# Kernel optimization log

Measured on AMD Instinct MI355X. Metric: run time of the kernel, lower is better.

The kernel has to match this reference:

```python
import jax, jax.numpy as jnp
import numpy as np

LN_EPS = 1e-5
FD_EPS = 1e-3   # cfg.fd_eps
MAX_ITER = 2    # cfg.max_iter; early-exit on tol is a host-side .item() check in torch, omitted for jit (fixed iterations)


def _block(w1, b1, w2, b2, g, beta, x):
    # pre-LN MLP residual block: x + W2 @ gelu(W1 @ LN(x))
    mu = jnp.mean(x, axis=-1, keepdims=True)
    var = jnp.var(x, axis=-1, keepdims=True)
    xn = (x - mu) * jax.lax.rsqrt(var + LN_EPS) * g + beta
    h = jax.nn.gelu(xn @ w1 + b1)
    return x + h @ w2 + b2

# apply block_l to state_l for all l at once: (L,B,T,C) -> (L,B,T,C)
_vblock = jax.vmap(_block, in_axes=(0, 0, 0, 0, 0, 0, 0))


def _scan_solve(As, bs):
    # solve x_l = A_l * x_{l-1} + b_l with x_0 = b_0 (A_0 unused), O(log L)
    def combine(e1, e2):
        A1, c1 = e1
        A2, c2 = e2
        return A2 * A1, A2 * c1 + c2
    _, xs = jax.lax.associative_scan(combine, (As, bs), axis=0)
    return xs


def setup_inputs() -> dict:
    key = jax.random.key(0)
    ks = jax.random.split(key, 3)
    L, B, T, C, F = 12, 2, 512, 768, 3072
    return {
        "x0": jax.random.normal(ks[0], (B, T, C), jnp.float32),
        "w1": jax.random.normal(ks[1], (L, C, F), jnp.float32) * 0.02,
        "b1": jnp.zeros((L, F), jnp.float32),
        "w2": jax.random.normal(ks[2], (L, F, C), jnp.float32) * 0.02,
        "b2": jnp.zeros((L, C), jnp.float32),
        "g": jnp.ones((L, C), jnp.float32),
        "beta": jnp.zeros((L, C), jnp.float32),
    }


def reference(x0, w1, b1, w2, b2, g, beta):
    L = w1.shape[0]
    # picard warmstart: states[l+1] = block_l(x0) (computed under torch.no_grad)
    warm = jax.lax.stop_gradient(
        _vblock(w1, b1, w2, b2, g, beta, jnp.broadcast_to(x0, (L,) + x0.shape)))
    states = jnp.concatenate([x0[None], warm], axis=0)  # (L+1, B, T, C)
    key = jax.random.key(42)
    for it in range(MAX_ITER):
        # residuals r_l = block_l(x_l) - x_{l+1}
        outs = _vblock(w1, b1, w2, b2, g, beta, states[:-1])
        res = outs - states[1:]
        # quasi-DEER FD diagonal Jacobian (Rademacher probe, under no_grad)
        sg = jax.lax.stop_gradient(states[:-1])
        v = jnp.sign(jax.random.normal(jax.random.fold_in(key, it), sg.shape, jnp.float32))
        op = _vblock(w1, b1, w2, b2, g, beta, sg + FD_EPS * v)
        om = _vblock(w1, b1, w2, b2, g, beta, sg - FD_EPS * v)
        diag_J = jax.lax.stop_gradient((op - om) / (2.0 * FD_EPS) * v)
        # damping k=0 for quasi-deer -> A_l = diag_J_l, b_l = r_l
        delta = _scan_solve(diag_J, res)  # (L, B, T, C)
        states = states.at[1:].add(delta)
    return states[-1]
```

## Files before the change

kernel.cpp:

```cpp
#include <hip/hip_runtime.h>
#include <hip/hip_bf16.h>
#include <stdint.h>


typedef __bf16 bf16;
typedef __bf16 bf16x8 __attribute__((ext_vector_type(8)));
typedef float f32x4 __attribute__((ext_vector_type(4)));

#define LAY_A   1572864
#define LAY_W   2359296
#define LAY_Z   6291456
#define LAY_S   786432

#define GLDS16(gp, lp) __builtin_amdgcn_global_load_lds(                      \
    (const __attribute__((address_space(1))) void*)(gp),                      \
    (__attribute__((address_space(3))) void*)(lp), 16, 0, 0)

#define WAITVM(N) asm volatile("s_waitcnt vmcnt(%0)" :: "n"(N) : "memory")
#define CFENCE()  asm volatile("" ::: "memory")

#define TF_ROT(x0, x1, n) { x0 += x1; x1 = (x1 << n) | (x1 >> (32 - n)); x1 ^= x0; }
__host__ __device__ __forceinline__ void threefry2x32(
    uint32_t k1, uint32_t k2, uint32_t c0, uint32_t c1, uint32_t& o0, uint32_t& o1)
{
  const uint32_t ks2 = k1 ^ k2 ^ 0x1BD11BDAu;
  uint32_t x0 = c0 + k1, x1 = c1 + k2;
  TF_ROT(x0,x1,13) TF_ROT(x0,x1,15) TF_ROT(x0,x1,26) TF_ROT(x0,x1,6)
  x0 += k2;  x1 += ks2 + 1u;
  TF_ROT(x0,x1,17) TF_ROT(x0,x1,29) TF_ROT(x0,x1,16) TF_ROT(x0,x1,24)
  x0 += ks2; x1 += k1 + 2u;
  TF_ROT(x0,x1,13) TF_ROT(x0,x1,15) TF_ROT(x0,x1,26) TF_ROT(x0,x1,6)
  x0 += k1;  x1 += k2 + 3u;
  TF_ROT(x0,x1,17) TF_ROT(x0,x1,29) TF_ROT(x0,x1,16) TF_ROT(x0,x1,24)
  x0 += k2;  x1 += ks2 + 4u;
  TF_ROT(x0,x1,13) TF_ROT(x0,x1,15) TF_ROT(x0,x1,26) TF_ROT(x0,x1,6)
  x0 += ks2; x1 += k1 + 5u;
  o0 = x0; o1 = x1;
}

__global__ __launch_bounds__(256) void transpose_kernel(
    const float* __restrict__ w, bf16* __restrict__ wt, int R, int Cc)
{
  __shared__ float tile[32][33];
  const int l = blockIdx.z;
  const float* wp = w + (size_t)l * R * Cc;
  bf16* wtp = wt + (size_t)l * R * Cc;
  const int c0 = blockIdx.x * 32;
  const int r0 = blockIdx.y * 32;
  const int tx = threadIdx.x & 31, ty = threadIdx.x >> 5;
  #pragma unroll
  for (int q = 0; q < 4; ++q)
    tile[ty + q * 8][tx] = wp[(size_t)(r0 + ty + q * 8) * Cc + c0 + tx];
  __syncthreads();
  #pragma unroll
  for (int q = 0; q < 4; ++q)
    wtp[(size_t)(c0 + ty + q * 8) * R + r0 + tx] = (bf16)tile[tx][ty + q * 8];
}

__device__ __forceinline__ void gelu2(float z, float& h, float& dg)
{
  const float z2 = z * z;
  const float u = 0.7978845608028654f * (z + 0.044715f * z2 * z);
  const float t = tanhf(u);
  h = 0.5f * z * (1.f + t);
  dg = 0.5f * (1.f + t) +
       0.5f * z * (1.f - t * t) * 0.7978845608028654f * (1.f + 0.134145f * z2);
}

template <int MODE>
__global__ __launch_bounds__(512, 2) void gemm_dbuf(
    const bf16* __restrict__ Abase, const bf16* __restrict__ Bbase,
    bf16* __restrict__ zh_out, float* __restrict__ states,
    float* __restrict__ resA, const bf16* __restrict__ vbuf,
    const float* __restrict__ bias1, const float* __restrict__ b2,
    const float* __restrict__ x0, int Mt)
{
  constexpr int LDAB  = (MODE <= 1) ? 768 : 3072;
  constexpr int NKT   = (MODE <= 1) ? 12 : 48;
  constexpr int NTN   = (MODE <= 1) ? 12 : ((MODE == 2) ? 3 : 6);
  constexpr int TN    = (MODE == 3) ? 128 : 256;
  constexpr int NFRAG = TN / 64;
  constexpr int ACH   = 32;
  constexpr int BCH   = TN / 8;
  constexpr int NCH   = (ACH + BCH) / 8;
  constexpr int ABYTES = 32768;
  constexpr int TILE  = ABYTES + BCH * 1024;
  constexpr size_t LSA = (MODE <= 1) ? LAY_A : LAY_Z;

  __shared__ __align__(16) char lds[2][TILE];

  const int tid  = threadIdx.x;
  const int lane = tid & 63;
  const int wid  = tid >> 6;
  const int wr   = wid >> 2;
  const int wc   = wid & 3;
  const int r16  = lane & 15;
  const int hi   = lane >> 4;

  const int nwg = gridDim.x;
  const int bid = blockIdx.x;
  const int swz = (bid & 7) * (nwg >> 3) + (bid >> 3);
  const int per_l = Mt * NTN;
  const int l   = swz / per_l;
  const int rr_ = swz - l * per_l;
  const int mt  = rr_ / NTN;
  const int nt  = rr_ - mt * NTN;
  const int m0  = mt * 256, n0 = nt * TN;

  const bf16* A = Abase + (size_t)l * LSA   + (size_t)m0 * LDAB;
  const bf16* B = Bbase + (size_t)l * LAY_W + (size_t)n0 * LDAB;

  const int rsub = lane >> 3;
  const int c8   = (lane & 7) ^ rsub;
  auto STAGE = [&](char* dst, int kt) {
    #pragma unroll
    for (int j = 0; j < NCH; ++j) {
      const int chunk = j * 8 + wid;
      if (chunk < ACH) {
        const int row = chunk * 8 + rsub;
        GLDS16(A + (size_t)row * LDAB + kt + c8 * 8, dst + chunk * 1024);
      } else {
        const int row = (chunk - ACH) * 8 + rsub;
        GLDS16(B + (size_t)row * LDAB + kt + c8 * 8,
               dst + ABYTES + (chunk - ACH) * 1024);
      }
    }
  };

  f32x4 acc[8][NFRAG] = {};

  auto COMPUTE = [&](const char* buf) {
    const char* As = buf;
    const char* Bs = buf + ABYTES;
    const int xw = (r16 & 7) << 4;
    #pragma unroll
    for (int kk = 0; kk < 2; ++kk) {
      const int cb = kk * 64;
      bf16x8 bfrag[NFRAG];
      #pragma unroll
      for (int ni = 0; ni < NFRAG; ++ni) {
        const int rn = wc * (TN / 4) + ni * 16 + r16;
        bfrag[ni] = *(const bf16x8*)(Bs + rn * 128 + ((cb + hi * 16) ^ xw));
      }
      #pragma unroll
      for (int mh = 0; mh < 2; ++mh) {
        bf16x8 afrag[4];
        #pragma unroll
        for (int q = 0; q < 4; ++q) {
          const int rm = wr * 128 + (mh * 4 + q) * 16 + r16;
          afrag[q] = *(const bf16x8*)(As + rm * 128 + ((cb + hi * 16) ^ xw));
        }
        #pragma unroll
        for (int q = 0; q < 4; ++q)
          #pragma unroll
          for (int ni = 0; ni < NFRAG; ++ni)
            acc[mh * 4 + q][ni] = __builtin_amdgcn_mfma_f32_16x16x32_bf16(
                afrag[q], bfrag[ni], acc[mh * 4 + q][ni], 0, 0, 0);
      }
    }
  };

  STAGE(lds[0], 0);
  STAGE(lds[1], 64);
  WAITVM(NCH);
  __builtin_amdgcn_s_barrier();
  CFENCE();
  COMPUTE(lds[0]);
  #pragma unroll 1
  for (int t = 1; t < NKT; ++t) {
    CFENCE();
    __builtin_amdgcn_s_barrier();
    CFENCE();
    if (t + 1 < NKT) {
      STAGE(lds[(t + 1) & 1], (t + 1) * 64);
      WAITVM(NCH);
    } else {
      WAITVM(0);
    }
    __builtin_amdgcn_s_barrier();
    CFENCE();
    COMPUTE(lds[t & 1]);
  }

  #pragma unroll
  for (int mi = 0; mi < 8; ++mi) {
    const int row0 = m0 + wr * 128 + mi * 16 + hi * 4;
    #pragma unroll
    for (int ni = 0; ni < NFRAG; ++ni) {
      const int col = n0 + wc * (TN / 4) + ni * 16 + r16;
      if (MODE == 0) {
        bf16* Cp = zh_out + (size_t)l * LAY_Z;
        const float bias = bias1[l * 3072 + col];
        #pragma unroll
        for (int r = 0; r < 4; ++r) {
          float h, dg;
          gelu2(acc[mi][ni][r] + bias, h, dg);
          Cp[(size_t)(row0 + r) * 3072 + col] = (bf16)h;
        }
      } else if (MODE == 1) {
        bf16* Cp = zh_out + (size_t)l * LAY_Z;
        const float bias = bias1[l * 3072 + col];
        #pragma unroll
        for (int p = 0; p < 2; ++p) {
          float h, dg;
          gelu2(acc[mi][ni][2 * p] + bias, h, dg);
          Cp[(size_t)(row0 + 2 * p) * 3072 + col] = (bf16)h;
          Cp[(size_t)(row0 + 2 * p + 1) * 3072 + col] =
              (bf16)(dg * acc[mi][ni][2 * p + 1]);
        }
      } else if (MODE == 2) {
        float* Sp = states + (size_t)(l + 1) * LAY_S;
        const float bb = b2[l * 768 + col];
        #pragma unroll
        for (int r = 0; r < 4; ++r)
          Sp[(size_t)(row0 + r) * 768 + col] =
              acc[mi][ni][r] + bb + x0[(size_t)(row0 + r) * 768 + col];
      } else {
        float* Rp = resA + (size_t)l * LAY_A;
        const float bb = b2[l * 768 + col];
        #pragma unroll
        for (int p = 0; p < 2; ++p) {
          const int tok = (row0 >> 1) + p;
          Rp[(size_t)tok * 768 + col] = acc[mi][ni][2 * p] + bb
              + states[(size_t)l * LAY_S + (size_t)tok * 768 + col]
              - states[(size_t)(l + 1) * LAY_S + (size_t)tok * 768 + col];
          const float vv = (float)vbuf[(size_t)l * LAY_S +
                                       (size_t)tok * 768 + col];
          Rp[LAY_S + (size_t)tok * 768 + col] =
              1.0f + acc[mi][ni][2 * p + 1] * vv;
        }
      }
    }
  }
}

__global__ __launch_bounds__(256) void ln_warm_kernel(
    const float* __restrict__ x0, const float* __restrict__ g,
    const float* __restrict__ beta, bf16* __restrict__ a_buf)
{
  const int row = blockIdx.x * 4 + (threadIdx.x >> 6);
  const int lane = threadIdx.x & 63;
  const float* x = x0 + (size_t)row * 768;
  float xl[12];
  float s1 = 0.f, s2 = 0.f;
  #pragma unroll
  for (int j = 0; j < 12; ++j) {
    float t = x[lane + 64 * j];
    xl[j] = t; s1 += t; s2 += t * t;
  }
  #pragma unroll
  for (int off = 1; off < 64; off <<= 1) {
    s1 += __shfl_xor(s1, off);
    s2 += __shfl_xor(s2, off);
  }
  const float mu = s1 * (1.f / 768.f);
  const float var = s2 * (1.f / 768.f) - mu * mu;
  const float rstd = rsqrtf(var + 1e-5f);
  float xh[12];
  #pragma unroll
  for (int j = 0; j < 12; ++j) xh[j] = (xl[j] - mu) * rstd;
  for (int l = 0; l < 12; ++l) {
    const float* gp = g + l * 768;
    const float* bp = beta + l * 768;
    bf16* ap = a_buf + (size_t)l * LAY_A + (size_t)row * 768;
    #pragma unroll
    for (int j = 0; j < 12; ++j) {
      const int c = lane + 64 * j;
      ap[c] = (bf16)(xh[j] * gp[c] + bp[c]);
    }
  }
}

__global__ __launch_bounds__(256) void ln_iter_kernel(
    const float* __restrict__ states, bf16* __restrict__ vbuf,
    const float* __restrict__ g, const float* __restrict__ beta,
    bf16* __restrict__ a_buf, uint32_t k1, uint32_t k2)
{
  const int gr = blockIdx.x * 4 + (threadIdx.x >> 6);
  const int l = gr >> 10;
  const int row = gr & 1023;
  const int lane = threadIdx.x & 63;
  const float* x = states + (size_t)l * LAY_S + (size_t)row * 768;
  bf16* vp = vbuf + (size_t)gr * 768;
  float xl[12], vl[12];
  float s1 = 0.f, s2 = 0.f, sv = 0.f, sxv = 0.f;
  #pragma unroll
  for (int j = 0; j < 12; ++j) {
    const int c = lane + 64 * j;
    const float t = x[c];
    uint32_t o0, o1;
    threefry2x32(k1, k2, 0u, (uint32_t)gr * 768u + (uint32_t)c, o0, o1);
    const float u = ((o0 ^ o1) & 0x80000000u) ? 1.0f : -1.0f;
    vp[c] = (bf16)u;
    xl[j] = t; vl[j] = u;
    s1 += t; s2 += t * t; sv += u; sxv += t * u;
  }
  #pragma unroll
  for (int off = 1; off < 64; off <<= 1) {
    s1 += __shfl_xor(s1, off); s2 += __shfl_xor(s2, off);
    sv += __shfl_xor(sv, off); sxv += __shfl_xor(sxv, off);
  }
  const float mu = s1 * (1.f / 768.f);
  const float var = s2 * (1.f / 768.f) - mu * mu;
  const float rstd = rsqrtf(var + 1e-5f);
  const float mv = sv * (1.f / 768.f);
  const float mhv = rstd * (sxv * (1.f / 768.f) - mu * mv);
  const float* gp = g + l * 768;
  const float* bp = beta + l * 768;
  bf16* ap = a_buf + (size_t)l * LAY_A + (size_t)(2 * row) * 768;
  bf16* dp = ap + 768;
  #pragma unroll
  for (int j = 0; j < 12; ++j) {
    const int c = lane + 64 * j;
    const float xh = (xl[j] - mu) * rstd;
    ap[c] = (bf16)(xh * gp[c] + bp[c]);
    dp[c] = (bf16)(rstd * ((vl[j] - mv) - xh * mhv) * gp[c]);
  }
}

__global__ __launch_bounds__(256) void scan_kernel(
    const float* __restrict__ resA, float* __restrict__ states)
{
  const size_t i = (size_t)blockIdx.x * 256 + threadIdx.x;
  float run = resA[i];
  states[LAY_S + i] += run;
  #pragma unroll
  for (int l = 1; l < 12; ++l) {
    const float b  = resA[(size_t)l * LAY_A + i];
    const float Aa = resA[(size_t)l * LAY_A + LAY_S + i];
    run = b + Aa * run;
    states[(size_t)(l + 1) * LAY_S + i] += run;
  }
}

extern "C" void kernel_launch(void* const* d_in, const int* in_sizes, int n_in,
                              void* d_out, int out_size, void* d_ws, size_t ws_size,
                              hipStream_t stream)
{
  const float* x0   = (const float*)d_in[0];
  const float* w1   = (const float*)d_in[1];
  const float* b1   = (const float*)d_in[2];
  const float* w2   = (const float*)d_in[3];
  const float* b2   = (const float*)d_in[4];
  const float* g    = (const float*)d_in[5];
  const float* beta = (const float*)d_in[6];

  char* ws = (char*)d_ws;
  size_t off = 0;
  auto alloc = [&](size_t bytes) -> void* {
    void* p = ws + off;
    off += (bytes + 255) & ~(size_t)255;
    return p;
  };
  bf16*  w1t    = (bf16*)alloc(2ULL * 12 * LAY_W);
  bf16*  w2t    = (bf16*)alloc(2ULL * 12 * LAY_W);
  float* states = (float*)alloc(4ULL * 13 * LAY_S);
  bf16*  a_buf  = (bf16*)alloc(2ULL * 12 * LAY_A);
  bf16*  zh     = (bf16*)alloc(2ULL * 12 * LAY_Z);
  float* resA   = (float*)alloc(4ULL * 12 * LAY_A);
  bf16*  vbuf   = (bf16*)alloc(2ULL * 12 * LAY_S);

  transpose_kernel<<<dim3(96, 24, 12), 256, 0, stream>>>(w1, w1t, 768, 3072);
  transpose_kernel<<<dim3(24, 96, 12), 256, 0, stream>>>(w2, w2t, 3072, 768);
  hipMemcpyAsync(states, x0, 4ULL * LAY_S, hipMemcpyDeviceToDevice, stream);

  ln_warm_kernel<<<256, 256, 0, stream>>>(x0, g, beta, a_buf);
  gemm_dbuf<0><<<576, 512, 0, stream>>>(a_buf, w1t, zh, states, resA, vbuf,
                                        b1, b2, x0, 4);
  gemm_dbuf<2><<<144, 512, 0, stream>>>(zh, w2t, nullptr, states, resA, vbuf,
                                        b1, b2, x0, 4);

  for (int it = 0; it < 2; ++it) {
    uint32_t k1, k2;
    threefry2x32(0u, 42u, 0u, (uint32_t)it, k1, k2);
    ln_iter_kernel<<<3072, 256, 0, stream>>>(states, vbuf, g, beta, a_buf,
                                             k1, k2);
    gemm_dbuf<1><<<1152, 512, 0, stream>>>(a_buf, w1t, zh, states, resA, vbuf,
                                           b1, b2, x0, 8);
    gemm_dbuf<3><<<576, 512, 0, stream>>>(zh, w2t, nullptr, states, resA, vbuf,
                                          b1, b2, x0, 8);
    scan_kernel<<<3072, 256, 0, stream>>>(resA, states);
  }

  hipMemcpyAsync(d_out, states + 12ULL * LAY_S, 4ULL * LAY_S,
                 hipMemcpyDeviceToDevice, stream);
}
```

Baseline: 1.130 ms.

## Use 256x128 tiles for all GEMM modes with triple-buffered LDS pipeline

Every GEMM mode now uses a 256x128 output tile with a 4x2 wave layout (64x64 per wave). Grid sizes double for the modes that previously used 256-wide tiles. The LDS double buffer becomes a triple buffer that prefetches two k-tiles ahead, aiming to hide global load latency better and to raise occupancy and wave counts through smaller accumulator arrays. The cost is more A-tile reloads per output and more total LDS per block.

```diff
diff --git a/kernel.cpp b/kernel.cpp
--- a/kernel.cpp
+++ b/kernel.cpp
@@ -77,23 +77,21 @@
 {
   constexpr int LDAB  = (MODE <= 1) ? 768 : 3072;
   constexpr int NKT   = (MODE <= 1) ? 12 : 48;
-  constexpr int NTN   = (MODE <= 1) ? 12 : ((MODE == 2) ? 3 : 6);
-  constexpr int TN    = (MODE == 3) ? 128 : 256;
-  constexpr int NFRAG = TN / 64;
+  constexpr int NTN   = (MODE <= 1) ? 24 : 6;
   constexpr int ACH   = 32;
-  constexpr int BCH   = TN / 8;
+  constexpr int BCH   = 16;
   constexpr int NCH   = (ACH + BCH) / 8;
   constexpr int ABYTES = 32768;
   constexpr int TILE  = ABYTES + BCH * 1024;
   constexpr size_t LSA = (MODE <= 1) ? LAY_A : LAY_Z;
 
-  __shared__ __align__(16) char lds[2][TILE];
+  __shared__ __align__(16) char lds[3][TILE];
 
   const int tid  = threadIdx.x;
   const int lane = tid & 63;
   const int wid  = tid >> 6;
-  const int wr   = wid >> 2;
-  const int wc   = wid & 3;
+  const int wr   = wid >> 1;
+  const int wc   = wid & 1;
   const int r16  = lane & 15;
   const int hi   = lane >> 4;
 
@@ -105,7 +103,7 @@
   const int rr_ = swz - l * per_l;
   const int mt  = rr_ / NTN;
   const int nt  = rr_ - mt * NTN;
-  const int m0  = mt * 256, n0 = nt * TN;
+  const int m0  = mt * 256, n0 = nt * 128;
 
   const bf16* A = Abase + (size_t)l * LSA   + (size_t)m0 * LDAB;
   const bf16* B = Bbase + (size_t)l * LAY_W + (size_t)n0 * LDAB;
@@ -127,7 +125,7 @@
     }
   };
 
-  f32x4 acc[8][NFRAG] = {};
+  f32x4 acc[4][4] = {};
 
   auto COMPUTE = [&](const char* buf) {
     const char* As = buf;
@@ -136,58 +134,53 @@
     #pragma unroll
     for (int kk = 0; kk < 2; ++kk) {
       const int cb = kk * 64;
-      bf16x8 bfrag[NFRAG];
+      bf16x8 bfrag[4];
       #pragma unroll
-      for (int ni = 0; ni < NFRAG; ++ni) {
-        const int rn = wc * (TN / 4) + ni * 16 + r16;
+      for (int ni = 0; ni < 4; ++ni) {
+        const int rn = wc * 64 + ni * 16 + r16;
         bfrag[ni] = *(const bf16x8*)(Bs + rn * 128 + ((cb + hi * 16) ^ xw));
       }
+      bf16x8 afrag[4];
       #pragma unroll
-      for (int mh = 0; mh < 2; ++mh) {
-        bf16x8 afrag[4];
-        #pragma unroll
-        for (int q = 0; q < 4; ++q) {
-          const int rm = wr * 128 + (mh * 4 + q) * 16 + r16;
-          afrag[q] = *(const bf16x8*)(As + rm * 128 + ((cb + hi * 16) ^ xw));
-        }
-        #pragma unroll
-        for (int q = 0; q < 4; ++q)
-          #pragma unroll
-          for (int ni = 0; ni < NFRAG; ++ni)
-            acc[mh * 4 + q][ni] = __builtin_amdgcn_mfma_f32_16x16x32_bf16(
-                afrag[q], bfrag[ni], acc[mh * 4 + q][ni], 0, 0, 0);
+      for (int q = 0; q < 4; ++q) {
+        const int rm = wr * 64 + q * 16 + r16;
+        afrag[q] = *(const bf16x8*)(As + rm * 128 + ((cb + hi * 16) ^ xw));
       }
+      #pragma unroll
+      for (int q = 0; q < 4; ++q)
+        #pragma unroll
+        for (int ni = 0; ni < 4; ++ni)
+          acc[q][ni] = __builtin_amdgcn_mfma_f32_16x16x32_bf16(
+              afrag[q], bfrag[ni], acc[q][ni], 0, 0, 0);
     }
   };
 
   STAGE(lds[0], 0);
   STAGE(lds[1], 64);
-  WAITVM(NCH);
-  __builtin_amdgcn_s_barrier();
-  CFENCE();
-  COMPUTE(lds[0]);
   #pragma unroll 1
-  for (int t = 1; t < NKT; ++t) {
+  for (int t = 0; t < NKT; ++t) {
     CFENCE();
     __builtin_amdgcn_s_barrier();
     CFENCE();
-    if (t + 1 < NKT) {
-      STAGE(lds[(t + 1) & 1], (t + 1) * 64);
+    if (t + 2 < NKT) {
+      STAGE(lds[(t + 2) % 3], (t + 2) * 64);
+      WAITVM(2 * NCH);
+    } else if (t + 1 < NKT) {
       WAITVM(NCH);
     } else {
       WAITVM(0);
     }
     __builtin_amdgcn_s_barrier();
     CFENCE();
-    COMPUTE(lds[t & 1]);
-  }
-
-  #pragma unroll
-  for (int mi = 0; mi < 8; ++mi) {
-    const int row0 = m0 + wr * 128 + mi * 16 + hi * 4;
+    COMPUTE(lds[t % 3]);
+  }
+
+  #pragma unroll
+  for (int mi = 0; mi < 4; ++mi) {
+    const int row0 = m0 + wr * 64 + mi * 16 + hi * 4;
     #pragma unroll
-    for (int ni = 0; ni < NFRAG; ++ni) {
-      const int col = n0 + wc * (TN / 4) + ni * 16 + r16;
+    for (int ni = 0; ni < 4; ++ni) {
+      const int col = n0 + wc * 64 + ni * 16 + r16;
       if (MODE == 0) {
         bf16* Cp = zh_out + (size_t)l * LAY_Z;
         const float bias = bias1[l * 3072 + col];
@@ -365,9 +358,9 @@
   hipMemcpyAsync(states, x0, 4ULL * LAY_S, hipMemcpyDeviceToDevice, stream);
 
   ln_warm_kernel<<<256, 256, 0, stream>>>(x0, g, beta, a_buf);
-  gemm_dbuf<0><<<576, 512, 0, stream>>>(a_buf, w1t, zh, states, resA, vbuf,
-                                        b1, b2, x0, 4);
-  gemm_dbuf<2><<<144, 512, 0, stream>>>(zh, w2t, nullptr, states, resA, vbuf,
+  gemm_dbuf<0><<<1152, 512, 0, stream>>>(a_buf, w1t, zh, states, resA, vbuf,
+                                         b1, b2, x0, 4);
+  gemm_dbuf<2><<<288, 512, 0, stream>>>(zh, w2t, nullptr, states, resA, vbuf,
                                         b1, b2, x0, 4);
 
   for (int it = 0; it < 2; ++it) {
@@ -375,7 +368,7 @@
     threefry2x32(0u, 42u, 0u, (uint32_t)it, k1, k2);
     ln_iter_kernel<<<3072, 256, 0, stream>>>(states, vbuf, g, beta, a_buf,
                                              k1, k2);
-    gemm_dbuf<1><<<1152, 512, 0, stream>>>(a_buf, w1t, zh, states, resA, vbuf,
+    gemm_dbuf<1><<<2304, 512, 0, stream>>>(a_buf, w1t, zh, states, resA, vbuf,
                                            b1, b2, x0, 8);
     gemm_dbuf<3><<<576, 512, 0, stream>>>(zh, w2t, nullptr, states, resA, vbuf,
                                           b1, b2, x0, 8);
```

Measured after the change: 1.155 ms. 2.2% more time.
